# Optimization experiments

Hardware: AMD Instinct MI355X
Metric: run time of the kernel (lower is better)

Reference implementation:

```python
import jax, jax.numpy as jnp
import numpy as np

B, S, D = 2, 2048, 2048
H = 32
HD = D // H  # 64
EPS = 1e-4


def setup_inputs() -> dict:
    key = jax.random.key(0)
    ks = jax.random.split(key, 9)
    hidden_states = jax.random.normal(ks[0], (B, S, D), dtype=jnp.float32)
    # multiplicative causal mask
    attention_mask = jnp.tril(jnp.ones((S, S), dtype=jnp.float32))[None, None]
    scale = 0.02
    wq = jax.random.normal(ks[1], (D, D), dtype=jnp.float32) * scale
    wk = jax.random.normal(ks[2], (D, D), dtype=jnp.float32) * scale
    wv = jax.random.normal(ks[3], (D, D), dtype=jnp.float32) * scale
    wo = jax.random.normal(ks[4], (D, D), dtype=jnp.float32) * scale
    bq = jax.random.normal(ks[5], (D,), dtype=jnp.float32) * scale
    bk = jax.random.normal(ks[6], (D,), dtype=jnp.float32) * scale
    bv = jax.random.normal(ks[7], (D,), dtype=jnp.float32) * scale
    bo = jax.random.normal(ks[8], (D,), dtype=jnp.float32) * scale
    return {"hidden_states": hidden_states, "attention_mask": attention_mask,
            "wq": wq, "bq": bq, "wk": wk, "bk": bk, "wv": wv, "bv": bv,
            "wo": wo, "bo": bo}


def _split_heads(x):
    # [B, S, D] -> [B, H, S, HD]
    b, s, _ = x.shape
    return x.reshape(b, s, H, HD).transpose(0, 2, 1, 3)


def reference(hidden_states, attention_mask, wq, bq, wk, bk, wv, bv, wo, bo):
    scaling = HD ** -0.5
    q = (hidden_states @ wq.T + bq) * scaling
    k = hidden_states @ wk.T + bk
    v = hidden_states @ wv.T + bv
    q, k, v = _split_heads(q), _split_heads(k), _split_heads(v)
    # ELU+1 feature map, then sum-normalize over head dim
    q = jax.nn.elu(q) + 1.0
    k = jax.nn.elu(k) + 1.0
    q = q / (q.sum(-1, keepdims=True) + EPS)
    k = k / (k.sum(-1, keepdims=True) + EPS)
    # quadratic attention: [B, H, S, S]
    attn = jnp.einsum('bhsd,bhtd->bhst', q, k) * (HD ** -0.5)
    attn = attn * attention_mask  # multiplicative mask
    out = jnp.einsum('bhst,bhtd->bhsd', attn, v)  # [B, H, S, HD]
    out = out.transpose(0, 2, 1, 3).reshape(hidden_states.shape[0], -1, D)
    return out @ wo.T + bo
```

## Files before the change

kernel.cpp:

```cpp
#include <hip/hip_runtime.h>

typedef __bf16 bf16x8 __attribute__((ext_vector_type(8)));
typedef float f32x4 __attribute__((ext_vector_type(4)));

#define GLDS(g, l) __builtin_amdgcn_global_load_lds(                              \
    (const __attribute__((address_space(1))) void*)(g),                            \
    (__attribute__((address_space(3))) void*)(l), 16, 0, 0)

#define PHASE_FENCE_PRE()  __builtin_amdgcn_sched_barrier(0)
#define PHASE_FENCE_POST()                                     \
  asm volatile("s_waitcnt lgkmcnt(0)" ::: "memory");           \
  __builtin_amdgcn_sched_barrier(0)

__device__ __forceinline__ unsigned short f2bf(float f) {
  unsigned int u = __builtin_bit_cast(unsigned int, f);
  u = (u + 0x7fffu + ((u >> 16) & 1u)) >> 16;
  return (unsigned short)u;
}
__device__ __forceinline__ float bf2f(unsigned short h) {
  unsigned int u = ((unsigned int)h) << 16;
  return __builtin_bit_cast(float, u);
}

__global__ __launch_bounds__(256) void cvt_f32_bf16(
    const float* __restrict__ in, unsigned short* __restrict__ out, int n4) {
  int i = blockIdx.x * 256 + threadIdx.x;
  if (i < n4) {
    float4 v = ((const float4*)in)[i];
    ushort4 o;
    o.x = f2bf(v.x); o.y = f2bf(v.y); o.z = f2bf(v.z); o.w = f2bf(v.w);
    ((ushort4*)out)[i] = o;
  }
}

__global__ __launch_bounds__(256) void cvt_w4(
    const float* __restrict__ w0, const float* __restrict__ w1,
    const float* __restrict__ w2, const float* __restrict__ w3,
    unsigned short* __restrict__ out) {
  const int y = blockIdx.y;
  const float* src = (y == 0) ? w0 : (y == 1) ? w1 : (y == 2) ? w2 : w3;
  const int i = blockIdx.x * 256 + threadIdx.x;
  float4 v = ((const float4*)src)[i];
  ushort4 o;
  o.x = f2bf(v.x); o.y = f2bf(v.y); o.z = f2bf(v.z); o.w = f2bf(v.w);
  ((ushort4*)(out + (size_t)y * 4194304))[i] = o;
}

__global__ __launch_bounds__(512, 2) void gemm384_qkv(
    const unsigned short* __restrict__ A, const unsigned short* __restrict__ Bw,
    const float* __restrict__ bq, const float* __restrict__ bk, const float* __restrict__ bv,
    unsigned short* __restrict__ oQ, unsigned short* __restrict__ oK,
    unsigned short* __restrict__ oV) {
  constexpr int K = 2048, NT = 32;
  __shared__ unsigned short lds[81920];
  const int tid = threadIdx.x, lane = tid & 63, wid = tid >> 6;
  const int wm = wid >> 1, wn = wid & 1;

  const int g0 = blockIdx.x;
  const int wg = (g0 & 7) * 32 + (g0 >> 3);
  const int chunk = wg >> 5, l = wg & 31;
  const int bx = (chunk & 3) * 4 + (l >> 3);
  const int by = (chunk >> 2) * 8 + (l & 7);

  const int rloc = tid >> 3;
  const size_t gcoff = (size_t)(((lane & 7) ^ (lane >> 3)) << 3);
  const unsigned short* gA = A  + (size_t)(by * 256 + rloc) * K + gcoff;
  const unsigned short* gB = Bw + (size_t)(bx * 384 + rloc) * K + gcoff;

#define ABu(b) ((b) * 16384)
#define BBu(b) (32768 + (b) * 24576)
#define STAGE_A(c, b) GLDS(gA + (size_t)(c) * 64 * K, lds + ABu(b) + (c) * 4096 + wid * 512)
#define STAGE_B(c, b) GLDS(gB + (size_t)(c) * 64 * K, lds + BBu(b) + (c) * 4096 + wid * 512)

  const int arow = (wm * 64 + (lane & 15)) * 64;
  const int brow = (wn * 192 + (lane & 15)) * 64;
  const int sw0 = (((lane >> 4)) ^ (lane & 7)) << 3;
  const int sw1 = ((4 + (lane >> 4)) ^ (lane & 7)) << 3;

  f32x4 acc[4][12] = {};

  STAGE_A(0, 0); STAGE_A(1, 0); STAGE_A(2, 0); STAGE_A(3, 0);
  STAGE_B(0, 0); STAGE_B(1, 0); STAGE_B(2, 0); STAGE_B(3, 0); STAGE_B(4, 0); STAGE_B(5, 0);
  gA += 64; gB += 64;
  asm volatile("s_waitcnt vmcnt(0)" ::: "memory");
  __builtin_amdgcn_s_barrier();

  for (int t = 0; t < NT; ++t) {
    const int Ab = ABu(t & 1) + arow;
    const int Bb = BBu(t & 1) + brow;
    const int sb = (t + 1) & 1;
    const bool st = (t + 1 < NT);
    bf16x8 Af[4], Bf[6];

    if (st) { STAGE_B(0, sb); STAGE_B(1, sb); STAGE_B(2, sb); }
#pragma unroll
    for (int m = 0; m < 4; ++m) Af[m] = *(const bf16x8*)&lds[Ab + m * 1024 + sw0];
#pragma unroll
    for (int n = 0; n < 6; ++n) Bf[n] = *(const bf16x8*)&lds[Bb + n * 1024 + sw0];
    PHASE_FENCE_PRE();
    __builtin_amdgcn_s_barrier();
    PHASE_FENCE_POST();
    __builtin_amdgcn_s_setprio(1);
#pragma unroll
    for (int m = 0; m < 4; ++m)
#pragma unroll
      for (int n = 0; n < 6; ++n)
        acc[m][n] = __builtin_amdgcn_mfma_f32_16x16x32_bf16(Af[m], Bf[n], acc[m][n], 0, 0, 0);
    __builtin_amdgcn_s_setprio(0);
    __builtin_amdgcn_s_barrier();

    if (st) { STAGE_B(3, sb); STAGE_B(4, sb); STAGE_B(5, sb); }
#pragma unroll
    for (int n = 0; n < 6; ++n) Bf[n] = *(const bf16x8*)&lds[Bb + (n + 6) * 1024 + sw0];
    PHASE_FENCE_PRE();
    __builtin_amdgcn_s_barrier();
    PHASE_FENCE_POST();
    __builtin_amdgcn_s_setprio(1);
#pragma unroll
    for (int m = 0; m < 4; ++m)
#pragma unroll
      for (int n = 0; n < 6; ++n)
        acc[m][n + 6] = __builtin_amdgcn_mfma_f32_16x16x32_bf16(Af[m], Bf[n], acc[m][n + 6], 0, 0, 0);
    __builtin_amdgcn_s_setprio(0);
    __builtin_amdgcn_s_barrier();

    if (st) { STAGE_A(0, sb); STAGE_A(1, sb); STAGE_A(2, sb); STAGE_A(3, sb); }
#pragma unroll
    for (int m = 0; m < 4; ++m) Af[m] = *(const bf16x8*)&lds[Ab + m * 1024 + sw1];
#pragma unroll
    for (int n = 0; n < 6; ++n) Bf[n] = *(const bf16x8*)&lds[Bb + n * 1024 + sw1];
    PHASE_FENCE_PRE();
    __builtin_amdgcn_s_barrier();
    PHASE_FENCE_POST();
    __builtin_amdgcn_s_setprio(1);
#pragma unroll
    for (int m = 0; m < 4; ++m)
#pragma unroll
      for (int n = 0; n < 6; ++n)
        acc[m][n] = __builtin_amdgcn_mfma_f32_16x16x32_bf16(Af[m], Bf[n], acc[m][n], 0, 0, 0);
    __builtin_amdgcn_s_setprio(0);
    __builtin_amdgcn_s_barrier();

#pragma unroll
    for (int n = 0; n < 6; ++n) Bf[n] = *(const bf16x8*)&lds[Bb + (n + 6) * 1024 + sw1];
    PHASE_FENCE_PRE();
    __builtin_amdgcn_s_barrier();
    PHASE_FENCE_POST();
    __builtin_amdgcn_s_setprio(1);
#pragma unroll
    for (int m = 0; m < 4; ++m)
#pragma unroll
      for (int n = 0; n < 6; ++n)
        acc[m][n + 6] = __builtin_amdgcn_mfma_f32_16x16x32_bf16(Af[m], Bf[n], acc[m][n + 6], 0, 0, 0);
    __builtin_amdgcn_s_setprio(0);
    if (st) {
      gA += 64; gB += 64;
      asm volatile("s_waitcnt vmcnt(0)" ::: "memory");
    }
    __builtin_amdgcn_s_barrier();
  }

  const int head0 = bx * 6 + wn * 3;
#pragma unroll
  for (int g = 0; g < 3; ++g) {
    const int head = head0 + g;
    const int type = head >> 5;
    const int h = head & 31;
    const float* bias = (type == 0) ? bq : (type == 1) ? bk : bv;
    unsigned short* dst = (type == 0) ? oQ : (type == 1) ? oK : oV;
    float bv4[4];
#pragma unroll
    for (int j = 0; j < 4; ++j) bv4[j] = bias[h * 64 + j * 16 + (lane & 15)];
#pragma unroll
    for (int m = 0; m < 4; ++m) {
#pragma unroll
      for (int r = 0; r < 4; ++r) {
        const int row = by * 256 + wm * 64 + m * 16 + ((lane >> 4) << 2) + r;
        const int bb = row >> 11, s = row & 2047;
        float e[4];
        float loc = 0.f;
#pragma unroll
        for (int j = 0; j < 4; ++j) {
          float v = acc[m][g * 4 + j][r] + bv4[j];
          if (type == 0) v *= 0.125f;
          if (type < 2) v = (v > 0.f) ? (v + 1.f) : __expf(v);
          e[j] = v; loc += v;
        }
        if (type < 2) {
#pragma unroll
          for (int off = 1; off < 16; off <<= 1) loc += __shfl_xor(loc, off, 64);
          const float inv = 1.f / (loc + 1e-4f);
#pragma unroll
          for (int j = 0; j < 4; ++j) e[j] *= inv;
        }
        const size_t base = ((size_t)((bb << 5) + h) * 2048 + s) * 64;
#pragma unroll
        for (int j = 0; j < 4; ++j) dst[base + j * 16 + (lane & 15)] = f2bf(e[j]);
      }
    }
  }
#undef ABu
#undef BBu
#undef STAGE_A
#undef STAGE_B
}

__global__ __launch_bounds__(512, 2) void gemm128_wo(
    const unsigned short* __restrict__ A, const unsigned short* __restrict__ Bw,
    const float* __restrict__ b0, float* __restrict__ C) {
  constexpr int K = 2048, NT = 32;
  __shared__ unsigned short lds[73728];
  const int tid = threadIdx.x, lane = tid & 63, wid = tid >> 6;
  const int wm = wid >> 2, wn = wid & 3;

  const int g0 = blockIdx.x;
  const int wg = (g0 & 7) * 32 + (g0 >> 3);
  const int l = wg % 32;
  const int chunk = wg / 32;
  const int bx2 = (chunk % 4) * 2 + l / 16;
  const int by2 = (chunk / 4) * 16 + l % 16;

  const int rloc = wid * 8 + (lane >> 3);
  const size_t gcoff = (size_t)(((lane & 7) ^ (lane >> 3)) << 3);
  const unsigned short* gA[2];
  const unsigned short* gB[4];
#pragma unroll
  for (int c = 0; c < 2; ++c) gA[c] = A + (size_t)(by2 * 128 + c * 64 + rloc) * K + gcoff;
#pragma unroll
  for (int c = 0; c < 4; ++c) gB[c] = Bw + (size_t)(bx2 * 256 + c * 64 + rloc) * K + gcoff;

  int aoff[4][2], boff[4][2];
#pragma unroll
  for (int m = 0; m < 4; ++m)
#pragma unroll
    for (int kk = 0; kk < 2; ++kk) {
      aoff[m][kk] = (wm * 64 + m * 16 + (lane & 15)) * 64 +
                    ((((kk << 2) + (lane >> 4)) ^ (lane & 7)) << 3);
      boff[m][kk] = (wn * 64 + m * 16 + (lane & 15)) * 64 +
                    ((((kk << 2) + (lane >> 4)) ^ (lane & 7)) << 3);
    }

  f32x4 acc[4][4] = {};

#define AB(b) ((b) * 8192)
#define BB(b) (24576 + (b) * 16384)
#define STAGE_A(c, b) GLDS(gA[c], lds + AB(b) + (c) * 4096 + wid * 512)
#define STAGE_B(c, b) GLDS(gB[c], lds + BB(b) + (c) * 4096 + wid * 512)

  STAGE_A(0, 0); STAGE_A(1, 0); STAGE_B(0, 0); STAGE_B(1, 0); STAGE_B(2, 0); STAGE_B(3, 0);
#pragma unroll
  for (int c = 0; c < 2; ++c) gA[c] += 64;
#pragma unroll
  for (int c = 0; c < 4; ++c) gB[c] += 64;
  STAGE_A(0, 1); STAGE_A(1, 1); STAGE_B(0, 1); STAGE_B(1, 1); STAGE_B(2, 1); STAGE_B(3, 1);
#pragma unroll
  for (int c = 0; c < 2; ++c) gA[c] += 64;
#pragma unroll
  for (int c = 0; c < 4; ++c) gB[c] += 64;
  asm volatile("s_waitcnt vmcnt(6)" ::: "memory");
  __builtin_amdgcn_s_barrier();

  for (int t = 0; t < NT; ++t) {
    const int b = t % 3;
    const int sb = (t + 2) % 3;
    const bool doStage = (t + 2 < NT);

    if (doStage) { STAGE_A(0, sb); STAGE_A(1, sb); STAGE_B(0, sb); STAGE_B(1, sb); }
    bf16x8 af[4], bfr[4];
#pragma unroll
    for (int m = 0; m < 4; ++m) af[m] = *(const bf16x8*)&lds[AB(b) + aoff[m][0]];
#pragma unroll
    for (int n = 0; n < 4; ++n) bfr[n] = *(const bf16x8*)&lds[BB(b) + boff[n][0]];
    PHASE_FENCE_PRE();
    __builtin_amdgcn_s_barrier();
    PHASE_FENCE_POST();
    __builtin_amdgcn_s_setprio(1);
#pragma unroll
    for (int m = 0; m < 4; ++m)
#pragma unroll
      for (int n = 0; n < 4; ++n)
        acc[m][n] = __builtin_amdgcn_mfma_f32_16x16x32_bf16(af[m], bfr[n], acc[m][n], 0, 0, 0);
    __builtin_amdgcn_s_setprio(0);
    __builtin_amdgcn_s_barrier();

    if (doStage) { STAGE_B(2, sb); STAGE_B(3, sb); }
#pragma unroll
    for (int c = 0; c < 2; ++c) gA[c] += 64;
#pragma unroll
    for (int c = 0; c < 4; ++c) gB[c] += 64;
#pragma unroll
    for (int m = 0; m < 4; ++m) af[m] = *(const bf16x8*)&lds[AB(b) + aoff[m][1]];
#pragma unroll
    for (int n = 0; n < 4; ++n) bfr[n] = *(const bf16x8*)&lds[BB(b) + boff[n][1]];
    PHASE_FENCE_PRE();
    __builtin_amdgcn_s_barrier();
    PHASE_FENCE_POST();
    __builtin_amdgcn_s_setprio(1);
#pragma unroll
    for (int m = 0; m < 4; ++m)
#pragma unroll
      for (int n = 0; n < 4; ++n)
        acc[m][n] = __builtin_amdgcn_mfma_f32_16x16x32_bf16(af[m], bfr[n], acc[m][n], 0, 0, 0);
    __builtin_amdgcn_s_setprio(0);
    if (t < NT - 1) {
      if (doStage) asm volatile("s_waitcnt vmcnt(6)" ::: "memory");
      else         asm volatile("s_waitcnt vmcnt(0)" ::: "memory");
    }
    __builtin_amdgcn_s_barrier();
  }

#pragma unroll
  for (int n = 0; n < 4; ++n) {
    const int col = bx2 * 256 + wn * 64 + n * 16 + (lane & 15);
    const float bv_ = b0[col];
#pragma unroll
    for (int m = 0; m < 4; ++m) {
      const int row0 = by2 * 128 + wm * 64 + m * 16 + ((lane >> 4) << 2);
#pragma unroll
      for (int r = 0; r < 4; ++r)
        C[(size_t)(row0 + r) * 2048 + col] = acc[m][n][r] + bv_;
    }
  }
#undef AB
#undef BB
#undef STAGE_A
#undef STAGE_B
}

__global__ __launch_bounds__(256) void chunk_state(
    const unsigned short* __restrict__ Kn, const unsigned short* __restrict__ Vn,
    unsigned short* __restrict__ stT) {
  __shared__ unsigned short Kt[64 * 72];
  __shared__ unsigned short Vt[64 * 72];
  const int c = blockIdx.x, bh = blockIdx.y;
  const int tid = threadIdx.x, lane = tid & 63, wid = tid >> 6;
  const size_t base = (size_t)bh * 2048 * 64 + (size_t)c * 64 * 64;
#pragma unroll
  for (int i = 0; i < 16; ++i) {
    const int ii = i * 256 + tid;
    const int t = ii >> 6, d = ii & 63;
    Kt[d * 72 + t] = Kn[base + ii];
    Vt[d * 72 + t] = Vn[base + ii];
  }
  __syncthreads();
  f32x4 acc[4] = {};
#pragma unroll
  for (int ks = 0; ks < 2; ++ks) {
    const int ko = ks * 32 + (lane >> 4) * 8;
    bf16x8 a = *(const bf16x8*)&Vt[(wid * 16 + (lane & 15)) * 72 + ko];
#pragma unroll
    for (int ej = 0; ej < 4; ++ej) {
      bf16x8 bb = *(const bf16x8*)&Kt[(ej * 16 + (lane & 15)) * 72 + ko];
      acc[ej] = __builtin_amdgcn_mfma_f32_16x16x32_bf16(a, bb, acc[ej], 0, 0, 0);
    }
  }
  const size_t obase = ((size_t)bh * 32 + c) * 4096;
#pragma unroll
  for (int ej = 0; ej < 4; ++ej) {
    const int e = ej * 16 + (lane & 15);
    const int d0 = wid * 16 + ((lane >> 4) << 2);
#pragma unroll
    for (int r = 0; r < 4; ++r)
      stT[obase + (size_t)(d0 + r) * 64 + e] = f2bf(acc[ej][r]);
  }
}

__global__ __launch_bounds__(256) void prefix_state(
    const unsigned short* __restrict__ stT, unsigned short* __restrict__ cumT) {
  const int g = blockIdx.x * 256 + threadIdx.x;
  const int bh = g >> 12, e = g & 4095;
  float run = 0.f;
  for (int c = 0; c < 32; ++c) {
    const size_t idx = (((size_t)bh * 32 + c) << 12) + e;
    const float v = bf2f(stT[idx]);
    cumT[idx] = f2bf(run);
    run += v;
  }
}

__global__ __launch_bounds__(256) void attn_intra(
    const unsigned short* __restrict__ Qn, const unsigned short* __restrict__ Kn,
    const unsigned short* __restrict__ Vn, const unsigned short* __restrict__ cumT,
    unsigned short* __restrict__ aout) {
  __shared__ unsigned short Qs[64 * 72];
  __shared__ unsigned short Ks[64 * 72];
  __shared__ unsigned short Vt[64 * 72];
  __shared__ unsigned short St[64 * 72];
  __shared__ unsigned short Ps[64 * 72];
  const int c = blockIdx.x, bh = blockIdx.y;
  const int tid = threadIdx.x, lane = tid & 63, wid = tid >> 6;
  const size_t base = (size_t)bh * 2048 * 64 + (size_t)c * 64 * 64;
  const size_t sbase = ((size_t)bh * 32 + c) * 4096;
#pragma unroll
  for (int i = 0; i < 16; ++i) {
    const int ii = i * 256 + tid;
    const int t = ii >> 6, d = ii & 63;
    Qs[t * 72 + d] = Qn[base + ii];
    Ks[t * 72 + d] = Kn[base + ii];
    Vt[d * 72 + t] = Vn[base + ii];
    St[t * 72 + d] = cumT[sbase + ii];
  }
  __syncthreads();
  f32x4 sacc[4] = {};
#pragma unroll
  for (int ks = 0; ks < 2; ++ks) {
    const int ko = ks * 32 + (lane >> 4) * 8;
    bf16x8 a = *(const bf16x8*)&Qs[(wid * 16 + (lane & 15)) * 72 + ko];
#pragma unroll
    for (int tj = 0; tj < 4; ++tj) {
      bf16x8 bb = *(const bf16x8*)&Ks[(tj * 16 + (lane & 15)) * 72 + ko];
      sacc[tj] = __builtin_amdgcn_mfma_f32_16x16x32_bf16(a, bb, sacc[tj], 0, 0, 0);
    }
  }
#pragma unroll
  for (int tj = 0; tj < 4; ++tj) {
    const int t = tj * 16 + (lane & 15);
    const int s0 = wid * 16 + ((lane >> 4) << 2);
#pragma unroll
    for (int r = 0; r < 4; ++r) {
      const float v = (t <= s0 + r) ? sacc[tj][r] : 0.f;
      Ps[(s0 + r) * 72 + t] = f2bf(v);
    }
  }
  __syncthreads();
  f32x4 oacc[4] = {};
#pragma unroll
  for (int ks = 0; ks < 2; ++ks) {
    const int ko = ks * 32 + (lane >> 4) * 8;
    bf16x8 a = *(const bf16x8*)&Ps[(wid * 16 + (lane & 15)) * 72 + ko];
    bf16x8 a2 = *(const bf16x8*)&Qs[(wid * 16 + (lane & 15)) * 72 + ko];
#pragma unroll
    for (int dj = 0; dj < 4; ++dj) {
      bf16x8 bv_ = *(const bf16x8*)&Vt[(dj * 16 + (lane & 15)) * 72 + ko];
      oacc[dj] = __builtin_amdgcn_mfma_f32_16x16x32_bf16(a, bv_, oacc[dj], 0, 0, 0);
      bf16x8 bs_ = *(const bf16x8*)&St[(dj * 16 + (lane & 15)) * 72 + ko];
      oacc[dj] = __builtin_amdgcn_mfma_f32_16x16x32_bf16(a2, bs_, oacc[dj], 0, 0, 0);
    }
  }
  const int b = bh >> 5, h = bh & 31;
#pragma unroll
  for (int dj = 0; dj < 4; ++dj) {
    const int d = dj * 16 + (lane & 15);
    const int s0 = wid * 16 + ((lane >> 4) << 2);
#pragma unroll
    for (int r = 0; r < 4; ++r) {
      const size_t row = (size_t)(b * 2048 + c * 64 + s0 + r);
      aout[row * 2048 + h * 64 + d] = f2bf(0.125f * oacc[dj][r]);
    }
  }
}

extern "C" void kernel_launch(void* const* d_in, const int* in_sizes, int n_in,
                              void* d_out, int out_size, void* d_ws, size_t ws_size,
                              hipStream_t stream) {
  const float* hs = (const float*)d_in[0];
  const float* wq = (const float*)d_in[2];
  const float* bq = (const float*)d_in[3];
  const float* wk = (const float*)d_in[4];
  const float* bk = (const float*)d_in[5];
  const float* wv = (const float*)d_in[6];
  const float* bv = (const float*)d_in[7];
  const float* wo = (const float*)d_in[8];
  const float* bo = (const float*)d_in[9];
  float* out = (float*)d_out;
  char* ws = (char*)d_ws;

  unsigned short* hs_bf   = (unsigned short*)(ws);
  unsigned short* wall_bf = (unsigned short*)(ws + 16777216);
  unsigned short* Qn      = (unsigned short*)(ws + 50331648);
  unsigned short* Kn      = (unsigned short*)(ws + 67108864);
  unsigned short* Vn      = (unsigned short*)(ws + 83886080);
  unsigned short* stT     = (unsigned short*)(ws + 100663296);
  unsigned short* cumT    = (unsigned short*)(ws + 117440512);
  unsigned short* aout    = (unsigned short*)(ws + 134217728);

  cvt_f32_bf16<<<8192, 256, 0, stream>>>(hs, hs_bf, 2097152);
  cvt_w4<<<dim3(4096, 4), 256, 0, stream>>>(wq, wk, wv, wo, wall_bf);

  gemm384_qkv<<<256, 512, 0, stream>>>(hs_bf, wall_bf, bq, bk, bv, Qn, Kn, Vn);

  chunk_state<<<dim3(32, 64), 256, 0, stream>>>(Kn, Vn, stT);
  prefix_state<<<1024, 256, 0, stream>>>(stT, cumT);
  attn_intra<<<dim3(32, 64), 256, 0, stream>>>(Qn, Kn, Vn, cumT, aout);

  gemm128_wo<<<256, 512, 0, stream>>>(aout, wall_bf + 12582912, bo, out);
}
```

Baseline: 205.3 us.

## Retile QKV GEMM to 256x256 blocks with 2x4 wave layout

Replaces the 256x384 tile QKV projection GEMM with a 256x256 tile variant launched as 384 blocks. Each wave now owns a 128x64 output slice (one full head), and the LDS staging is rearranged into half-tiles loaded across four phases. The grid-to-tile mapping is also changed. The likely intent is to cut LDS footprint for better occupancy and to balance the 256 CUs with 384 tiles, at the cost of more A/B reloads per output and a different load/compute interleave.

```diff
diff --git a/kernel.cpp b/kernel.cpp
--- a/kernel.cpp
+++ b/kernel.cpp
@@ -46,161 +46,187 @@
   ((ushort4*)(out + (size_t)y * 4194304))[i] = o;
 }
 
-__global__ __launch_bounds__(512, 2) void gemm384_qkv(
+__global__ __launch_bounds__(512, 2) void gemm256_qkv(
     const unsigned short* __restrict__ A, const unsigned short* __restrict__ Bw,
     const float* __restrict__ bq, const float* __restrict__ bk, const float* __restrict__ bv,
     unsigned short* __restrict__ oQ, unsigned short* __restrict__ oK,
     unsigned short* __restrict__ oV) {
   constexpr int K = 2048, NT = 32;
-  __shared__ unsigned short lds[81920];
+  __shared__ unsigned short lds[65536];
   const int tid = threadIdx.x, lane = tid & 63, wid = tid >> 6;
-  const int wm = wid >> 1, wn = wid & 1;
+  const int wm = wid >> 2;
+  const int wn = wid & 3;
 
   const int g0 = blockIdx.x;
-  const int wg = (g0 & 7) * 32 + (g0 >> 3);
-  const int chunk = wg >> 5, l = wg & 31;
-  const int bx = (chunk & 3) * 4 + (l >> 3);
-  const int by = (chunk >> 2) * 8 + (l & 7);
-
-  const int rloc = tid >> 3;
-  const size_t gcoff = (size_t)(((lane & 7) ^ (lane >> 3)) << 3);
-  const unsigned short* gA = A  + (size_t)(by * 256 + rloc) * K + gcoff;
-  const unsigned short* gB = Bw + (size_t)(bx * 384 + rloc) * K + gcoff;
-
-#define ABu(b) ((b) * 16384)
-#define BBu(b) (32768 + (b) * 24576)
-#define STAGE_A(c, b) GLDS(gA + (size_t)(c) * 64 * K, lds + ABu(b) + (c) * 4096 + wid * 512)
-#define STAGE_B(c, b) GLDS(gB + (size_t)(c) * 64 * K, lds + BBu(b) + (c) * 4096 + wid * 512)
-
-  const int arow = (wm * 64 + (lane & 15)) * 64;
-  const int brow = (wn * 192 + (lane & 15)) * 64;
+  const int wg = (g0 & 7) * 48 + (g0 >> 3);
+  const int bx = wg / 16;
+  const int by = wg % 16;
+
+  const int srow = tid >> 3;
+  const size_t gsw = (size_t)(((lane & 7) ^ (srow & 7)) << 3);
+  const unsigned short* gA = A  + (size_t)(by * 256 + srow) * K + gsw;
+  const unsigned short* gB = Bw + (size_t)(bx * 256 + srow) * K + gsw;
+
+#define STAGE_A(b, h, tt)                                                                    \
+  do {                                                                                       \
+    GLDS(gA + (size_t)((h) * 128) * K + (size_t)(tt) * 64,                                   \
+         lds + ((b) * 2 + (h)) * 8192 + wid * 512);                                          \
+    GLDS(gA + (size_t)((h) * 128 + 64) * K + (size_t)(tt) * 64,                              \
+         lds + ((b) * 2 + (h)) * 8192 + 4096 + wid * 512);                                   \
+  } while (0)
+#define STAGE_B(b, h, tt)                                                                    \
+  do {                                                                                       \
+    GLDS(gB + (size_t)((h) * 128) * K + (size_t)(tt) * 64,                                   \
+         lds + 32768 + ((b) * 2 + (h)) * 8192 + wid * 512);                                  \
+    GLDS(gB + (size_t)((h) * 128 + 64) * K + (size_t)(tt) * 64,                              \
+         lds + 32768 + ((b) * 2 + (h)) * 8192 + 4096 + wid * 512);                           \
+  } while (0)
+
+  const int l15 = lane & 15;
   const int sw0 = (((lane >> 4)) ^ (lane & 7)) << 3;
   const int sw1 = ((4 + (lane >> 4)) ^ (lane & 7)) << 3;
-
-  f32x4 acc[4][12] = {};
-
-  STAGE_A(0, 0); STAGE_A(1, 0); STAGE_A(2, 0); STAGE_A(3, 0);
-  STAGE_B(0, 0); STAGE_B(1, 0); STAGE_B(2, 0); STAGE_B(3, 0); STAGE_B(4, 0); STAGE_B(5, 0);
-  gA += 64; gB += 64;
+  const int abase = wm * 8192;
+  const int bbase = 32768 + ((wn >> 1)) * 8192;
+  const int brow0 = ((wn & 1) * 64 + l15) * 64;
+
+  f32x4 acc[8][4] = {};
+  bf16x8 Af[8], Bf[4];
+
+  STAGE_A(0, 0, 0); STAGE_A(0, 1, 0); STAGE_B(0, 0, 0); STAGE_B(0, 1, 0);
   asm volatile("s_waitcnt vmcnt(0)" ::: "memory");
   __builtin_amdgcn_s_barrier();
 
   for (int t = 0; t < NT; ++t) {
-    const int Ab = ABu(t & 1) + arow;
-    const int Bb = BBu(t & 1) + brow;
-    const int sb = (t + 1) & 1;
+    const int b = t & 1, nb = b ^ 1;
     const bool st = (t + 1 < NT);
-    bf16x8 Af[4], Bf[6];
-
-    if (st) { STAGE_B(0, sb); STAGE_B(1, sb); STAGE_B(2, sb); }
-#pragma unroll
-    for (int m = 0; m < 4; ++m) Af[m] = *(const bf16x8*)&lds[Ab + m * 1024 + sw0];
-#pragma unroll
-    for (int n = 0; n < 6; ++n) Bf[n] = *(const bf16x8*)&lds[Bb + n * 1024 + sw0];
+    const int aA = (b * 2 + wm) * 8192 + l15 * 64;
+    const int aB = bbase + b * 16384 + brow0;
+
+    if (st) { STAGE_A(nb, 0, t + 1); STAGE_B(nb, 1, t + 1); }
+#pragma unroll
+    for (int mq = 0; mq < 4; ++mq) {
+      Af[mq * 2]     = *(const bf16x8*)&lds[aA + mq * 1024 + sw0];
+      Af[mq * 2 + 1] = *(const bf16x8*)&lds[aA + mq * 1024 + sw1];
+    }
+#pragma unroll
+    for (int nq = 0; nq < 2; ++nq) {
+      Bf[nq * 2]     = *(const bf16x8*)&lds[aB + nq * 1024 + sw0];
+      Bf[nq * 2 + 1] = *(const bf16x8*)&lds[aB + nq * 1024 + sw1];
+    }
     PHASE_FENCE_PRE();
     __builtin_amdgcn_s_barrier();
     PHASE_FENCE_POST();
     __builtin_amdgcn_s_setprio(1);
 #pragma unroll
-    for (int m = 0; m < 4; ++m)
-#pragma unroll
-      for (int n = 0; n < 6; ++n)
-        acc[m][n] = __builtin_amdgcn_mfma_f32_16x16x32_bf16(Af[m], Bf[n], acc[m][n], 0, 0, 0);
+    for (int mq = 0; mq < 4; ++mq)
+#pragma unroll
+      for (int nq = 0; nq < 2; ++nq)
+#pragma unroll
+        for (int kk = 0; kk < 2; ++kk)
+          acc[mq][nq] = __builtin_amdgcn_mfma_f32_16x16x32_bf16(
+              Af[mq * 2 + kk], Bf[nq * 2 + kk], acc[mq][nq], 0, 0, 0);
     __builtin_amdgcn_s_setprio(0);
     __builtin_amdgcn_s_barrier();
 
-    if (st) { STAGE_B(3, sb); STAGE_B(4, sb); STAGE_B(5, sb); }
-#pragma unroll
-    for (int n = 0; n < 6; ++n) Bf[n] = *(const bf16x8*)&lds[Bb + (n + 6) * 1024 + sw0];
+    if (st) STAGE_B(nb, 0, t + 1);
+#pragma unroll
+    for (int mq = 0; mq < 4; ++mq) {
+      Af[mq * 2]     = *(const bf16x8*)&lds[aA + 4096 + mq * 1024 + sw0];
+      Af[mq * 2 + 1] = *(const bf16x8*)&lds[aA + 4096 + mq * 1024 + sw1];
+    }
     PHASE_FENCE_PRE();
     __builtin_amdgcn_s_barrier();
     PHASE_FENCE_POST();
     __builtin_amdgcn_s_setprio(1);
 #pragma unroll
-    for (int m = 0; m < 4; ++m)
-#pragma unroll
-      for (int n = 0; n < 6; ++n)
-        acc[m][n + 6] = __builtin_amdgcn_mfma_f32_16x16x32_bf16(Af[m], Bf[n], acc[m][n + 6], 0, 0, 0);
+    for (int mq = 0; mq < 4; ++mq)
+#pragma unroll
+      for (int nq = 0; nq < 2; ++nq)
+#pragma unroll
+        for (int kk = 0; kk < 2; ++kk)
+          acc[4 + mq][nq] = __builtin_amdgcn_mfma_f32_16x16x32_bf16(
+              Af[mq * 2 + kk], Bf[nq * 2 + kk], acc[4 + mq][nq], 0, 0, 0);
     __builtin_amdgcn_s_setprio(0);
     __builtin_amdgcn_s_barrier();
 
-    if (st) { STAGE_A(0, sb); STAGE_A(1, sb); STAGE_A(2, sb); STAGE_A(3, sb); }
-#pragma unroll
-    for (int m = 0; m < 4; ++m) Af[m] = *(const bf16x8*)&lds[Ab + m * 1024 + sw1];
-#pragma unroll
-    for (int n = 0; n < 6; ++n) Bf[n] = *(const bf16x8*)&lds[Bb + n * 1024 + sw1];
+    if (st) STAGE_A(nb, 1, t + 1);
+#pragma unroll
+    for (int nq = 0; nq < 2; ++nq) {
+      Bf[nq * 2]     = *(const bf16x8*)&lds[aB + 2048 + nq * 1024 + sw0];
+      Bf[nq * 2 + 1] = *(const bf16x8*)&lds[aB + 2048 + nq * 1024 + sw1];
+    }
     PHASE_FENCE_PRE();
     __builtin_amdgcn_s_barrier();
     PHASE_FENCE_POST();
     __builtin_amdgcn_s_setprio(1);
 #pragma unroll
-    for (int m = 0; m < 4; ++m)
-#pragma unroll
-      for (int n = 0; n < 6; ++n)
-        acc[m][n] = __builtin_amdgcn_mfma_f32_16x16x32_bf16(Af[m], Bf[n], acc[m][n], 0, 0, 0);
+    for (int mq = 0; mq < 4; ++mq)
+#pragma unroll
+      for (int nq = 0; nq < 2; ++nq)
+#pragma unroll
+        for (int kk = 0; kk < 2; ++kk)
+          acc[4 + mq][2 + nq] = __builtin_amdgcn_mfma_f32_16x16x32_bf16(
+              Af[mq * 2 + kk], Bf[nq * 2 + kk], acc[4 + mq][2 + nq], 0, 0, 0);
     __builtin_amdgcn_s_setprio(0);
     __builtin_amdgcn_s_barrier();
 
 #pragma unroll
-    for (int n = 0; n < 6; ++n) Bf[n] = *(const bf16x8*)&lds[Bb + (n + 6) * 1024 + sw1];
+    for (int mq = 0; mq < 4; ++mq) {
+      Af[mq * 2]     = *(const bf16x8*)&lds[aA + mq * 1024 + sw0];
+      Af[mq * 2 + 1] = *(const bf16x8*)&lds[aA + mq * 1024 + sw1];
+    }
     PHASE_FENCE_PRE();
     __builtin_amdgcn_s_barrier();
     PHASE_FENCE_POST();
     __builtin_amdgcn_s_setprio(1);
 #pragma unroll
-    for (int m = 0; m < 4; ++m)
-#pragma unroll
-      for (int n = 0; n < 6; ++n)
-        acc[m][n + 6] = __builtin_amdgcn_mfma_f32_16x16x32_bf16(Af[m], Bf[n], acc[m][n + 6], 0, 0, 0);
+    for (int mq = 0; mq < 4; ++mq)
+#pragma unroll
+      for (int nq = 0; nq < 2; ++nq)
+#pragma unroll
+        for (int kk = 0; kk < 2; ++kk)
+          acc[mq][2 + nq] = __builtin_amdgcn_mfma_f32_16x16x32_bf16(
+              Af[mq * 2 + kk], Bf[nq * 2 + kk], acc[mq][2 + nq], 0, 0, 0);
     __builtin_amdgcn_s_setprio(0);
-    if (st) {
-      gA += 64; gB += 64;
-      asm volatile("s_waitcnt vmcnt(0)" ::: "memory");
-    }
-    __builtin_amdgcn_s_barrier();
-  }
-
-  const int head0 = bx * 6 + wn * 3;
-#pragma unroll
-  for (int g = 0; g < 3; ++g) {
-    const int head = head0 + g;
-    const int type = head >> 5;
-    const int h = head & 31;
-    const float* bias = (type == 0) ? bq : (type == 1) ? bk : bv;
-    unsigned short* dst = (type == 0) ? oQ : (type == 1) ? oK : oV;
-    float bv4[4];
-#pragma unroll
-    for (int j = 0; j < 4; ++j) bv4[j] = bias[h * 64 + j * 16 + (lane & 15)];
-#pragma unroll
-    for (int m = 0; m < 4; ++m) {
-#pragma unroll
-      for (int r = 0; r < 4; ++r) {
-        const int row = by * 256 + wm * 64 + m * 16 + ((lane >> 4) << 2) + r;
-        const int bb = row >> 11, s = row & 2047;
-        float e[4];
-        float loc = 0.f;
-#pragma unroll
-        for (int j = 0; j < 4; ++j) {
-          float v = acc[m][g * 4 + j][r] + bv4[j];
-          if (type == 0) v *= 0.125f;
-          if (type < 2) v = (v > 0.f) ? (v + 1.f) : __expf(v);
-          e[j] = v; loc += v;
-        }
-        if (type < 2) {
-#pragma unroll
-          for (int off = 1; off < 16; off <<= 1) loc += __shfl_xor(loc, off, 64);
-          const float inv = 1.f / (loc + 1e-4f);
-#pragma unroll
-          for (int j = 0; j < 4; ++j) e[j] *= inv;
-        }
-        const size_t base = ((size_t)((bb << 5) + h) * 2048 + s) * 64;
-#pragma unroll
-        for (int j = 0; j < 4; ++j) dst[base + j * 16 + (lane & 15)] = f2bf(e[j]);
+    if (st) asm volatile("s_waitcnt vmcnt(0)" ::: "memory");
+    __builtin_amdgcn_s_barrier();
+  }
+
+  const int head = bx * 4 + wn;
+  const int type = head >> 5;
+  const int h = head & 31;
+  const float* bias = (type == 0) ? bq : (type == 1) ? bk : bv;
+  unsigned short* dst = (type == 0) ? oQ : (type == 1) ? oK : oV;
+  float bv4[4];
+#pragma unroll
+  for (int n = 0; n < 4; ++n) bv4[n] = bias[h * 64 + n * 16 + l15];
+#pragma unroll
+  for (int m = 0; m < 8; ++m) {
+#pragma unroll
+    for (int r = 0; r < 4; ++r) {
+      const int row = by * 256 + wm * 128 + m * 16 + ((lane >> 4) << 2) + r;
+      const int bb = row >> 11, s = row & 2047;
+      float e[4];
+      float loc = 0.f;
+#pragma unroll
+      for (int n = 0; n < 4; ++n) {
+        float v = acc[m][n][r] + bv4[n];
+        if (type == 0) v *= 0.125f;
+        if (type < 2) v = (v > 0.f) ? (v + 1.f) : __expf(v);
+        e[n] = v; loc += v;
       }
-    }
-  }
-#undef ABu
-#undef BBu
+      if (type < 2) {
+#pragma unroll
+        for (int off = 1; off < 16; off <<= 1) loc += __shfl_xor(loc, off, 64);
+        const float inv = 1.f / (loc + 1e-4f);
+#pragma unroll
+        for (int n = 0; n < 4; ++n) e[n] *= inv;
+      }
+      const size_t base = ((size_t)((bb << 5) + h) * 2048 + s) * 64;
+#pragma unroll
+      for (int n = 0; n < 4; ++n) dst[base + n * 16 + l15] = f2bf(e[n]);
+    }
+  }
 #undef STAGE_A
 #undef STAGE_B
 }
@@ -477,7 +503,7 @@
   cvt_f32_bf16<<<8192, 256, 0, stream>>>(hs, hs_bf, 2097152);
   cvt_w4<<<dim3(4096, 4), 256, 0, stream>>>(wq, wk, wv, wo, wall_bf);
 
-  gemm384_qkv<<<256, 512, 0, stream>>>(hs_bf, wall_bf, bq, bk, bv, Qn, Kn, Vn);
+  gemm256_qkv<<<384, 512, 0, stream>>>(hs_bf, wall_bf, bq, bk, bv, Qn, Kn, Vn);
 
   chunk_state<<<dim3(32, 64), 256, 0, stream>>>(Kn, Vn, stT);
   prefix_state<<<1024, 256, 0, stream>>>(stT, cumT);
```

Result: slower. 237.7 us (+15.8%).
